# Optimization experiments

Hardware: AMD Instinct MI355X
Metric: run time of the kernel (lower is better)

Reference implementation:

```python
import jax, jax.numpy as jnp
import numpy as np

N_NODES = 100000
N_EDGES = 1600000  # random edges; self-loops appended -> 1.7M total
NFEATS, NHIDS, NCLASSES = 512, 256, 40


def _spmm(edge_row, edge_col, edge_val, dense):
    # out[r] += val * dense[c]  (COO spmm)
    msgs = edge_val[:, None] * dense[edge_col]           # [E, F]
    return jax.ops.segment_sum(msgs, edge_row, num_segments=N_NODES)


def setup_inputs() -> dict:
    key = jax.random.key(0)
    ks = jax.random.split(key, 8)
    x = jax.random.normal(ks[0], (N_NODES, NFEATS), dtype=jnp.float32)
    stdv1 = 1.0 / np.sqrt(NHIDS)
    W1 = jax.random.uniform(ks[1], (NFEATS, NHIDS), minval=-stdv1, maxval=stdv1, dtype=jnp.float32)
    b1 = jax.random.uniform(ks[2], (NHIDS,), minval=-stdv1, maxval=stdv1, dtype=jnp.float32)
    stdv2 = 1.0 / np.sqrt(NCLASSES)
    W2 = jax.random.uniform(ks[3], (NHIDS, NCLASSES), minval=-stdv2, maxval=stdv2, dtype=jnp.float32)
    b2 = jax.random.uniform(ks[4], (NCLASSES,), minval=-stdv2, maxval=stdv2, dtype=jnp.float32)

    # random adjacency edges + self-loops (normalized_adj does adj = I + adj)
    r = jax.random.randint(ks[5], (N_EDGES,), 0, N_NODES, dtype=jnp.int32)
    c = jax.random.randint(ks[6], (N_EDGES,), 0, N_NODES, dtype=jnp.int32)
    sl = jnp.arange(N_NODES, dtype=jnp.int32)
    edge_row = jnp.concatenate([r, sl])
    edge_col = jnp.concatenate([c, sl])
    raw_val = jnp.ones(edge_row.shape[0], dtype=jnp.float32)
    # deg = row-sum of (A + I); symmetric normalization D^-1/2 (A+I) D^-1/2
    deg = jax.ops.segment_sum(raw_val, edge_row, num_segments=N_NODES)
    dinv = jnp.power(deg, -0.5)
    dinv = jnp.where(jnp.isfinite(dinv), dinv, 0.0)
    edge_val = dinv[edge_row] * raw_val * dinv[edge_col]
    return {"x": x, "W1": W1, "b1": b1, "W2": W2, "b2": b2,
            "edge_row": edge_row, "edge_col": edge_col, "edge_val": edge_val}


def reference(x, W1, b1, W2, b2, edge_row, edge_col, edge_val):
    # layer 1: relu(spmm(adj, x@W1) + b1); dropout skipped (eval mode)
    h = jax.nn.relu(_spmm(edge_row, edge_col, edge_val, x @ W1) + b1)
    # layer 2: spmm(adj, h@W2) + b2
    out = _spmm(edge_row, edge_col, edge_val, h @ W2) + b2
    return out
```

## Files before the change

kernel.cpp:

```cpp
#include <hip/hip_runtime.h>
#include <hip/hip_bf16.h>


#define NFEATS 512
#define NHIDS  256
#define NCLS   40
#define NCLSP  64

typedef unsigned short ushort_t;
typedef unsigned int uint_t;
typedef __attribute__((ext_vector_type(8))) short frag8;
typedef __attribute__((ext_vector_type(4))) float floatx4;

__device__ __forceinline__ ushort_t f2b(float f) {
    uint_t u = __float_as_uint(f);
    uint_t r = (u + 0x7fffu + ((u >> 16) & 1u)) >> 16;
    return (ushort_t)r;
}
__device__ __forceinline__ float b2f(ushort_t b) {
    return __uint_as_float((uint_t)b << 16);
}


__global__ void hist_kernel(const int* __restrict__ row, int* __restrict__ cnt, int E) {
    int e = blockIdx.x * blockDim.x + threadIdx.x;
    if (e < E) atomicAdd(&cnt[row[e]], 1);
}

#define PS_T 256
#define PS_C 4
#define PS_CHUNK (PS_T * PS_C)

__global__ __launch_bounds__(PS_T) void scan_partial_kernel(const int* __restrict__ cnt,
                                                            int* __restrict__ blockSums, int N) {
    __shared__ int sm[PS_T];
    int t = threadIdx.x;
    int base = blockIdx.x * PS_CHUNK + t * PS_C;
    int s = 0;
    if (base + PS_C <= N) {
        int4 v = *(const int4*)(cnt + base);
        s = v.x + v.y + v.z + v.w;
    } else {
        for (int i = 0; i < PS_C; i++) if (base + i < N) s += cnt[base + i];
    }
    sm[t] = s;
    __syncthreads();
    for (int off = PS_T / 2; off > 0; off >>= 1) {
        if (t < off) sm[t] += sm[t + off];
        __syncthreads();
    }
    if (t == 0) blockSums[blockIdx.x] = sm[0];
}

#define SS_T 128
__global__ __launch_bounds__(SS_T) void scan_sums_kernel(int* __restrict__ blockSums, int B) {
    __shared__ int sm[SS_T];
    int t = threadIdx.x;
    int v = (t < B) ? blockSums[t] : 0;
    sm[t] = v;
    __syncthreads();
    for (int off = 1; off < SS_T; off <<= 1) {
        int x = (t >= off) ? sm[t - off] : 0;
        __syncthreads();
        sm[t] += x;
        __syncthreads();
    }
    if (t < B) blockSums[t] = sm[t] - v;
}

__global__ __launch_bounds__(PS_T) void scan_finalize_kernel(int* __restrict__ cnt,
                                                             const int* __restrict__ blockSums,
                                                             int* __restrict__ row_ptr, int N, int E) {
    __shared__ int sm[PS_T];
    int t = threadIdx.x;
    int base = blockIdx.x * PS_CHUNK + t * PS_C;
    int vals[PS_C];
    int s = 0;
#pragma unroll
    for (int i = 0; i < PS_C; i++) {
        int idx = base + i;
        vals[i] = (idx < N) ? cnt[idx] : 0;
        s += vals[i];
    }
    sm[t] = s;
    __syncthreads();
    for (int off = 1; off < PS_T; off <<= 1) {
        int x = (t >= off) ? sm[t - off] : 0;
        __syncthreads();
        sm[t] += x;
        __syncthreads();
    }
    int run = blockSums[blockIdx.x] + sm[t] - s;
#pragma unroll
    for (int i = 0; i < PS_C; i++) {
        int idx = base + i;
        if (idx < N) {
            row_ptr[idx] = run;
            run += vals[i];
            cnt[idx] = 0;
        }
    }
    if (blockIdx.x == 0 && t == 0) row_ptr[N] = E;
}

__global__ void scatter_kernel(const int* __restrict__ row, const int* __restrict__ col,
                               const float* __restrict__ val, const int* __restrict__ row_ptr,
                               int* __restrict__ fill, int2* __restrict__ cv, int E) {
    int e = blockIdx.x * blockDim.x + threadIdx.x;
    if (e < E) {
        int r = row[e];
        int p = row_ptr[r] + atomicAdd(&fill[r], 1);
        cv[p] = make_int2(col[e], __float_as_int(val[e]));
    }
}


__global__ void convert_w1(const float* __restrict__ W1, ushort_t* __restrict__ W1t) {
    int idx = blockIdx.x * 256 + threadIdx.x;
    int k = idx >> 8, n = idx & 255;
    W1t[n * 512 + k] = f2b(W1[idx]);
}

__global__ void convert_w2(const float* __restrict__ W2, ushort_t* __restrict__ W2t) {
    int idx = blockIdx.x * 256 + threadIdx.x;
    int n = idx >> 8, k = idx & 255;
    W2t[idx] = (n < NCLS) ? f2b(W2[k * NCLS + n]) : (ushort_t)0;
}


#define G1_BM 64

__global__ __launch_bounds__(256) void gemm1_kernel(const float* __restrict__ A,
                                                    const ushort_t* __restrict__ Bt,
                                                    ushort_t* __restrict__ H1, int M) {
    int tid  = threadIdx.x;
    int wave = tid >> 6, lane = tid & 63;
    int quad = lane >> 4, ln = lane & 15;
    int m0 = blockIdx.x * G1_BM;

    floatx4 acc[4][4] = {};

    const ushort_t* bbase = Bt + (size_t)(wave * 64 + ln) * NFEATS + quad * 8;

    const float* abase[4];
#pragma unroll
    for (int mt = 0; mt < 4; mt++) {
        int m = m0 + mt * 16 + ln;
        if (m > M - 1) m = M - 1;
        abase[mt] = A + (size_t)m * NFEATS + quad * 8;
    }

#pragma unroll
    for (int t = 0; t < NFEATS / 32; ++t) {
        frag8 af[4], bfr[4];
#pragma unroll
        for (int nt = 0; nt < 4; nt++)
            bfr[nt] = *(const frag8*)(bbase + (size_t)nt * 16 * NFEATS + t * 32);
#pragma unroll
        for (int mt = 0; mt < 4; mt++) {
            float4 lo = *(const float4*)(abase[mt] + t * 32);
            float4 hi = *(const float4*)(abase[mt] + t * 32 + 4);
            frag8 f;
            f[0] = (short)f2b(lo.x); f[1] = (short)f2b(lo.y);
            f[2] = (short)f2b(lo.z); f[3] = (short)f2b(lo.w);
            f[4] = (short)f2b(hi.x); f[5] = (short)f2b(hi.y);
            f[6] = (short)f2b(hi.z); f[7] = (short)f2b(hi.w);
            af[mt] = f;
        }
#pragma unroll
        for (int mt = 0; mt < 4; mt++)
#pragma unroll
            for (int nt = 0; nt < 4; nt++)
                acc[mt][nt] = __builtin_amdgcn_mfma_f32_16x16x32_bf16(af[mt], bfr[nt], acc[mt][nt], 0, 0, 0);
    }

#pragma unroll
    for (int mt = 0; mt < 4; mt++) {
#pragma unroll
        for (int i = 0; i < 4; i++) {
            int m = m0 + mt * 16 + quad * 4 + i;
            if (m < M) {
#pragma unroll
                for (int nt = 0; nt < 4; nt++) {
                    H1[(size_t)m * NHIDS + wave * 64 + nt * 16 + ln] = f2b(acc[mt][nt][i]);
                }
            }
        }
    }
}


__global__ __launch_bounds__(256) void spmm1_kernel(const int* __restrict__ row_ptr,
                                                    const int2* __restrict__ cv,
                                                    const ushort_t* __restrict__ H1,
                                                    const float* __restrict__ b1,
                                                    ushort_t* __restrict__ AGG, int N) {
    int wave = threadIdx.x >> 6, lane = threadIdx.x & 63;
    int r = blockIdx.x * 4 + wave;
    if (r >= N) return;
    int s = row_ptr[r], e = row_ptr[r + 1];
    float a0 = 0.f, a1 = 0.f, a2 = 0.f, a3 = 0.f;
    int j = s;
    for (; j + 3 < e; j += 4) {
        int2 p0 = cv[j];
        int2 p1 = cv[j + 1];
        int2 p2 = cv[j + 2];
        int2 p3 = cv[j + 3];
        ushort4 h0 = *(const ushort4*)(H1 + (size_t)p0.x * NHIDS + lane * 4);
        ushort4 h1 = *(const ushort4*)(H1 + (size_t)p1.x * NHIDS + lane * 4);
        ushort4 h2 = *(const ushort4*)(H1 + (size_t)p2.x * NHIDS + lane * 4);
        ushort4 h3 = *(const ushort4*)(H1 + (size_t)p3.x * NHIDS + lane * 4);
        float v0 = __int_as_float(p0.y), v1 = __int_as_float(p1.y);
        float v2 = __int_as_float(p2.y), v3 = __int_as_float(p3.y);
        a0 += v0 * b2f(h0.x); a1 += v0 * b2f(h0.y); a2 += v0 * b2f(h0.z); a3 += v0 * b2f(h0.w);
        a0 += v1 * b2f(h1.x); a1 += v1 * b2f(h1.y); a2 += v1 * b2f(h1.z); a3 += v1 * b2f(h1.w);
        a0 += v2 * b2f(h2.x); a1 += v2 * b2f(h2.y); a2 += v2 * b2f(h2.z); a3 += v2 * b2f(h2.w);
        a0 += v3 * b2f(h3.x); a1 += v3 * b2f(h3.y); a2 += v3 * b2f(h3.z); a3 += v3 * b2f(h3.w);
    }
    for (; j < e; j++) {
        int2 p0 = cv[j];
        ushort4 h0 = *(const ushort4*)(H1 + (size_t)p0.x * NHIDS + lane * 4);
        float v0 = __int_as_float(p0.y);
        a0 += v0 * b2f(h0.x); a1 += v0 * b2f(h0.y); a2 += v0 * b2f(h0.z); a3 += v0 * b2f(h0.w);
    }
    float4 bb = *(const float4*)(b1 + lane * 4);
    a0 += bb.x; a1 += bb.y; a2 += bb.z; a3 += bb.w;
    ushort4 o;
    o.x = f2b(a0 > 0.f ? a0 : 0.f);
    o.y = f2b(a1 > 0.f ? a1 : 0.f);
    o.z = f2b(a2 > 0.f ? a2 : 0.f);
    o.w = f2b(a3 > 0.f ? a3 : 0.f);
    *(ushort4*)&AGG[(size_t)r * NHIDS + lane * 4] = o;
}


__global__ __launch_bounds__(256) void gemm2_kernel(const ushort_t* __restrict__ AGG,
                                                    const ushort_t* __restrict__ W2t,
                                                    ushort_t* __restrict__ H2, int M) {
    int tid  = threadIdx.x;
    int wave = tid >> 6, lane = tid & 63;
    int quad = lane >> 4, ln = lane & 15;
    int m0 = blockIdx.x * 256 + wave * 64;

    floatx4 acc[4][4] = {};
    frag8 zf = {};

#pragma unroll
    for (int k0 = 0; k0 < NHIDS; k0 += 32) {
        frag8 af[4], bf[4];
#pragma unroll
        for (int mt = 0; mt < 4; mt++) {
            int m = m0 + mt * 16 + ln;
            af[mt] = (m < M) ? *(const frag8*)(AGG + (size_t)m * NHIDS + k0 + quad * 8) : zf;
        }
#pragma unroll
        for (int nt = 0; nt < 4; nt++)
            bf[nt] = *(const frag8*)(W2t + (size_t)(nt * 16 + ln) * NHIDS + k0 + quad * 8);
#pragma unroll
        for (int mt = 0; mt < 4; mt++)
#pragma unroll
            for (int nt = 0; nt < 4; nt++)
                acc[mt][nt] = __builtin_amdgcn_mfma_f32_16x16x32_bf16(af[mt], bf[nt], acc[mt][nt], 0, 0, 0);
    }
#pragma unroll
    for (int mt = 0; mt < 4; mt++) {
#pragma unroll
        for (int i = 0; i < 4; i++) {
            int m = m0 + mt * 16 + quad * 4 + i;
            if (m < M) {
#pragma unroll
                for (int nt = 0; nt < 4; nt++)
                    H2[(size_t)m * NCLSP + nt * 16 + ln] = f2b(acc[mt][nt][i]);
            }
        }
    }
}


__global__ __launch_bounds__(256) void spmm2_kernel(const int* __restrict__ row_ptr,
                                                    const int2* __restrict__ cv,
                                                    const ushort_t* __restrict__ H2,
                                                    const float* __restrict__ b2,
                                                    float* __restrict__ out, int N) {
    int wave = threadIdx.x >> 6, lane = threadIdx.x & 63;
    int half = lane >> 5, fl = lane & 31;
    int r = blockIdx.x * 8 + wave * 2 + half;
    if (r >= N) return;
    int s = row_ptr[r], e = row_ptr[r + 1];
    float a0 = 0.f, a1 = 0.f;
    int j = s;
    for (; j + 3 < e; j += 4) {
        int2 p0 = cv[j];
        int2 p1 = cv[j + 1];
        int2 p2 = cv[j + 2];
        int2 p3 = cv[j + 3];
        float v0 = __int_as_float(p0.y);
        float v1 = __int_as_float(p1.y);
        float v2 = __int_as_float(p2.y);
        float v3 = __int_as_float(p3.y);
        uint_t h0 = *(const uint_t*)(H2 + (size_t)p0.x * NCLSP + fl * 2);
        uint_t h1 = *(const uint_t*)(H2 + (size_t)p1.x * NCLSP + fl * 2);
        uint_t h2 = *(const uint_t*)(H2 + (size_t)p2.x * NCLSP + fl * 2);
        uint_t h3 = *(const uint_t*)(H2 + (size_t)p3.x * NCLSP + fl * 2);
        a0 += v0 * b2f((ushort_t)(h0 & 0xffff));
        a1 += v0 * b2f((ushort_t)(h0 >> 16));
        a0 += v1 * b2f((ushort_t)(h1 & 0xffff));
        a1 += v1 * b2f((ushort_t)(h1 >> 16));
        a0 += v2 * b2f((ushort_t)(h2 & 0xffff));
        a1 += v2 * b2f((ushort_t)(h2 >> 16));
        a0 += v3 * b2f((ushort_t)(h3 & 0xffff));
        a1 += v3 * b2f((ushort_t)(h3 >> 16));
    }
    for (; j < e; j++) {
        int2 p = cv[j];
        float v = __int_as_float(p.y);
        uint_t h = *(const uint_t*)(H2 + (size_t)p.x * NCLSP + fl * 2);
        a0 += v * b2f((ushort_t)(h & 0xffff));
        a1 += v * b2f((ushort_t)(h >> 16));
    }
    if (fl < NCLS / 2) {
        float2 o;
        o.x = a0 + b2[fl * 2];
        o.y = a1 + b2[fl * 2 + 1];
        *(float2*)(out + (size_t)r * NCLS + fl * 2) = o;
    }
}


static inline size_t align256(size_t x) { return (x + 255) & ~(size_t)255; }

extern "C" void kernel_launch(void* const* d_in, const int* in_sizes, int n_in,
                              void* d_out, int out_size, void* d_ws, size_t ws_size,
                              hipStream_t stream) {
    const float* x        = (const float*)d_in[0];
    const float* W1       = (const float*)d_in[1];
    const float* b1       = (const float*)d_in[2];
    const float* W2       = (const float*)d_in[3];
    const float* b2       = (const float*)d_in[4];
    const int*   edge_row = (const int*)d_in[5];
    const int*   edge_col = (const int*)d_in[6];
    const float* edge_val = (const float*)d_in[7];
    float* out = (float*)d_out;

    int N = in_sizes[0] / NFEATS;
    int E = in_sizes[5];

    char* w = (char*)d_ws;
    size_t off = 0;
    ushort_t* H1   = (ushort_t*)(w + off); off += align256((size_t)N * NHIDS * 2);
    ushort_t* AGG  = (ushort_t*)(w + off); off += align256((size_t)N * NHIDS * 2);
    ushort_t* H2   = (ushort_t*)(w + off); off += align256((size_t)N * NCLSP * 2);
    ushort_t* W1t  = (ushort_t*)(w + off); off += align256((size_t)NHIDS * NFEATS * 2);
    ushort_t* W2t  = (ushort_t*)(w + off); off += align256((size_t)NCLSP * NHIDS * 2);
    int*      row_ptr = (int*)(w + off); off += align256((size_t)(N + 1) * 4);
    int*      cnt     = (int*)(w + off); off += align256((size_t)N * 4);
    int*      blockSums = (int*)(w + off); off += align256((size_t)SS_T * 4);
    int2*     cv      = (int2*)(w + off); off += align256((size_t)E * 8);

    int scanB = (N + PS_CHUNK - 1) / PS_CHUNK;

    hipMemsetAsync(cnt, 0, (size_t)N * 4, stream);
    hist_kernel<<<(E + 255) / 256, 256, 0, stream>>>(edge_row, cnt, E);
    convert_w1<<<(NFEATS * NHIDS) / 256, 256, 0, stream>>>(W1, W1t);
    convert_w2<<<(NCLSP * NHIDS) / 256, 256, 0, stream>>>(W2, W2t);
    scan_partial_kernel<<<scanB, PS_T, 0, stream>>>(cnt, blockSums, N);
    scan_sums_kernel<<<1, SS_T, 0, stream>>>(blockSums, scanB);
    scan_finalize_kernel<<<scanB, PS_T, 0, stream>>>(cnt, blockSums, row_ptr, N, E);
    scatter_kernel<<<(E + 255) / 256, 256, 0, stream>>>(edge_row, edge_col, edge_val,
                                                        row_ptr, cnt, cv, E);

    gemm1_kernel<<<(N + G1_BM - 1) / G1_BM, 256, 0, stream>>>(x, W1t, H1, N);
    spmm1_kernel<<<(N + 3) / 4, 256, 0, stream>>>(row_ptr, cv, H1, b1, AGG, N);

    gemm2_kernel<<<(N + 255) / 256, 256, 0, stream>>>(AGG, W2t, H2, N);
    spmm2_kernel<<<(N + 7) / 8, 256, 0, stream>>>(row_ptr, cv, H2, b2, out, N);
}
```

Baseline: 752.6 us.

## Stage GEMM1 A tiles via async global-to-LDS double buffering with packed bf16 convert

GEMM1 now copies fp32 A tiles into a double-buffered, XOR-swizzled LDS tile with global_load_lds, prefetching the next K-slab while MFMAs run on the current one. Previously each wave loaded A straight from global memory with redundant per-lane float4 reads. The manual round-to-nearest bf16 conversion is replaced with the hardware v_cvt_pk_bf16_f32 instruction. In exchange the kernel adds a __syncthreads per K step and uses more LDS. It also relies on the lane-to-address pattern of global_load_lds matching the swizzle layout.

```diff
diff --git a/kernel.cpp b/kernel.cpp
--- a/kernel.cpp
+++ b/kernel.cpp
@@ -11,6 +11,9 @@
 typedef unsigned int uint_t;
 typedef __attribute__((ext_vector_type(8))) short frag8;
 typedef __attribute__((ext_vector_type(4))) float floatx4;
+
+#define AS1C(p) ((__attribute__((address_space(1))) const void*)(p))
+#define AS3(p)  ((__attribute__((address_space(3))) void*)(p))
 
 __device__ __forceinline__ ushort_t f2b(float f) {
     uint_t u = __float_as_uint(f);
@@ -129,49 +132,75 @@
 
 
 #define G1_BM 64
+#define G1_BK 32
 
 __global__ __launch_bounds__(256) void gemm1_kernel(const float* __restrict__ A,
                                                     const ushort_t* __restrict__ Bt,
                                                     ushort_t* __restrict__ H1, int M) {
+    __shared__ float As[2][G1_BM * G1_BK];
     int tid  = threadIdx.x;
     int wave = tid >> 6, lane = tid & 63;
     int quad = lane >> 4, ln = lane & 15;
     int m0 = blockIdx.x * G1_BM;
 
+    int rloc0 = (wave * 2 + 0) * 8 + (lane >> 3);
+    int rloc1 = (wave * 2 + 1) * 8 + (lane >> 3);
+    int sslot = (lane & 7) ^ ((lane >> 3) & 7);
+    int gr0 = m0 + rloc0; if (gr0 > M - 1) gr0 = M - 1;
+    int gr1 = m0 + rloc1; if (gr1 > M - 1) gr1 = M - 1;
+    const float* src0 = A + (size_t)gr0 * NFEATS + sslot * 4;
+    const float* src1 = A + (size_t)gr1 * NFEATS + sslot * 4;
+    float* dst0 = &As[0][(wave * 2 + 0) * 256];
+    float* dst1 = &As[0][(wave * 2 + 1) * 256];
+    float* dst0b = &As[1][(wave * 2 + 0) * 256];
+    float* dst1b = &As[1][(wave * 2 + 1) * 256];
+
+    const ushort_t* bbase = Bt + (size_t)(wave * 64 + ln) * NFEATS + quad * 8;
+
     floatx4 acc[4][4] = {};
 
-    const ushort_t* bbase = Bt + (size_t)(wave * 64 + ln) * NFEATS + quad * 8;
-
-    const float* abase[4];
-#pragma unroll
-    for (int mt = 0; mt < 4; mt++) {
-        int m = m0 + mt * 16 + ln;
-        if (m > M - 1) m = M - 1;
-        abase[mt] = A + (size_t)m * NFEATS + quad * 8;
-    }
-
-#pragma unroll
-    for (int t = 0; t < NFEATS / 32; ++t) {
-        frag8 af[4], bfr[4];
+    __builtin_amdgcn_global_load_lds(AS1C(src0), AS3(dst0), 16, 0, 0);
+    __builtin_amdgcn_global_load_lds(AS1C(src1), AS3(dst1), 16, 0, 0);
+    __syncthreads();
+
+#pragma unroll 2
+    for (int t = 0; t < NFEATS / G1_BK; ++t) {
+        int cur = t & 1;
+        if (t < NFEATS / G1_BK - 1) {
+            const float* s0 = src0 + (t + 1) * G1_BK;
+            const float* s1 = src1 + (t + 1) * G1_BK;
+            if (cur == 0) {
+                __builtin_amdgcn_global_load_lds(AS1C(s0), AS3(dst0b), 16, 0, 0);
+                __builtin_amdgcn_global_load_lds(AS1C(s1), AS3(dst1b), 16, 0, 0);
+            } else {
+                __builtin_amdgcn_global_load_lds(AS1C(s0), AS3(dst0), 16, 0, 0);
+                __builtin_amdgcn_global_load_lds(AS1C(s1), AS3(dst1), 16, 0, 0);
+            }
+        }
+        frag8 bfr[4], af[4];
 #pragma unroll
         for (int nt = 0; nt < 4; nt++)
-            bfr[nt] = *(const frag8*)(bbase + (size_t)nt * 16 * NFEATS + t * 32);
+            bfr[nt] = *(const frag8*)(bbase + (size_t)nt * 16 * NFEATS + t * G1_BK);
 #pragma unroll
         for (int mt = 0; mt < 4; mt++) {
-            float4 lo = *(const float4*)(abase[mt] + t * 32);
-            float4 hi = *(const float4*)(abase[mt] + t * 32 + 4);
-            frag8 f;
-            f[0] = (short)f2b(lo.x); f[1] = (short)f2b(lo.y);
-            f[2] = (short)f2b(lo.z); f[3] = (short)f2b(lo.w);
-            f[4] = (short)f2b(hi.x); f[5] = (short)f2b(hi.y);
-            f[6] = (short)f2b(hi.z); f[7] = (short)f2b(hi.w);
-            af[mt] = f;
+            int R = mt * 16 + ln;
+            int sw = R & 7;
+            const float* base = &As[cur][R * G1_BK];
+            float4 lo = *(const float4*)(base + (((2 * quad)     ^ sw) * 4));
+            float4 hi = *(const float4*)(base + (((2 * quad + 1) ^ sw) * 4));
+            union { frag8 f; uint_t u[4]; } fu;
+            asm volatile("v_cvt_pk_bf16_f32 %0, %1, %2" : "=v"(fu.u[0]) : "v"(lo.x), "v"(lo.y));
+            asm volatile("v_cvt_pk_bf16_f32 %0, %1, %2" : "=v"(fu.u[1]) : "v"(lo.z), "v"(lo.w));
+            asm volatile("v_cvt_pk_bf16_f32 %0, %1, %2" : "=v"(fu.u[2]) : "v"(hi.x), "v"(hi.y));
+            asm volatile("v_cvt_pk_bf16_f32 %0, %1, %2" : "=v"(fu.u[3]) : "v"(hi.z), "v"(hi.w));
+            af[mt] = fu.f;
         }
 #pragma unroll
         for (int mt = 0; mt < 4; mt++)
 #pragma unroll
             for (int nt = 0; nt < 4; nt++)
                 acc[mt][nt] = __builtin_amdgcn_mfma_f32_16x16x32_bf16(af[mt], bfr[nt], acc[mt][nt], 0, 0, 0);
+        __syncthreads();
     }
 
 #pragma unroll
```

After: 688.2 us. -8.6%, faster.
